# Kernel tuning notes

Hardware: AMD Instinct MI355X
Metric: run time of the kernel (lower is better)

## Reference

```python
import jax, jax.numpy as jnp
import numpy as np

B, T, S = 64, 256, 512          # batch, decode steps, source length
IN, H, P, C = 512, 512, 256, 512  # in_size, rnn hidden, ctx_proj_size, ctx_size


def setup_inputs() -> dict:
    key = jax.random.key(0)
    ks = jax.random.split(key, 10)
    def n(k, sh, s=0.05):
        return jax.random.normal(k, sh, dtype=jnp.float32) * s
    return {
        "dec_input": n(ks[0], (B, T, IN), 1.0),
        "ctx": n(ks[1], (B, S, C), 1.0),
        "ctx_mask": jnp.ones((B, S), jnp.float32),
        # LSTMCell layer 0: input = in_size + ctx_proj_size (input feeding)
        "Wih0": n(ks[2], (4 * H, IN + P)),
        "Whh0": n(ks[3], (4 * H, H)),
        "bih0": jnp.zeros((4 * H,), jnp.float32),
        "bhh0": jnp.zeros((4 * H,), jnp.float32),
        # LSTMCell layer 1
        "Wih1": n(ks[4], (4 * H, H)),
        "Whh1": n(ks[5], (4 * H, H)),
        "bih1": jnp.zeros((4 * H,), jnp.float32),
        "bhh1": jnp.zeros((4 * H,), jnp.float32),
        # bilinear (Luong general) attention weight
        "Watt": n(ks[6], (H, C)),
        # ctx projection: Linear(rnn_size + att.out_features -> ctx_proj_size)
        "Wproj": n(ks[7], (P, H + C)),
        "bproj": jnp.zeros((P,), jnp.float32),
    }


def _lstm_cell(x, h, c, Wih, Whh, bih, bhh):
    # PyTorch LSTMCell gate order: i, f, g, o
    g = x @ Wih.T + bih + h @ Whh.T + bhh
    i, f, gg, o = jnp.split(g, 4, axis=-1)
    c_new = jax.nn.sigmoid(f) * c + jax.nn.sigmoid(i) * jnp.tanh(gg)
    h_new = jax.nn.sigmoid(o) * jnp.tanh(c_new)
    return h_new, c_new


def reference(dec_input, ctx, ctx_mask, Wih0, Whh0, bih0, bhh0,
              Wih1, Whh1, bih1, bhh1, Watt, Wproj, bproj):
    Bn = dec_input.shape[0]
    neg = (ctx_mask - 1.0) * 1e9  # additive mask: 0 where valid, -1e9 where pad

    def step(carry, x_t):
        h0, c0, h1, c1, feed = carry
        # input feeding at layer 0
        x = jnp.concatenate([x_t, feed], axis=1)
        h0, c0 = _lstm_cell(x, h0, c0, Wih0, Whh0, bih0, bhh0)
        h1, c1 = _lstm_cell(h0, h1, c1, Wih1, Whh1, bih1, bhh1)
        # attention on last layer (att_nth_layer == -1)
        q = h1 @ Watt                                   # [B, C]
        score = jnp.einsum('bc,bsc->bs', q, ctx) + neg  # [B, S]
        alpha = jax.nn.softmax(score, axis=-1)
        ectx = jnp.einsum('bs,bsc->bc', alpha, ctx)     # expected context [B, C]
        # ctx projection with tanh (scale_src = scale_tgt = 1.0)
        res = jnp.tanh(jnp.concatenate([h1, ectx], axis=1) @ Wproj.T + bproj)
        return (h0, c0, h1, c1, res), (res, alpha)

    z = lambda d: jnp.zeros((Bn, d), jnp.float32)
    init = (z(H), z(H), z(H), z(H), z(P))
    _, (dec_out, att_w) = jax.lax.scan(step, init, jnp.swapaxes(dec_input, 0, 1))
    # dec_output [B, T, P], attention weights [B, T, S]
    return jnp.swapaxes(dec_out, 0, 1), jnp.swapaxes(att_w, 0, 1)
```

## Files before the change

kernel.cpp:

```cpp
#include <hip/hip_runtime.h>
#include <math.h>

#define B  64
#define T  256
#define S  512
#define IN 512
#define H  512
#define P  256
#define C  512

typedef _Float16 f16x8 __attribute__((ext_vector_type(8)));
typedef float    f32x4 __attribute__((ext_vector_type(4)));
typedef unsigned short u16x8 __attribute__((ext_vector_type(8)));

#define MFMA16(a, b, c) __builtin_amdgcn_mfma_f32_16x16x32_f16(a, b, c, 0, 0, 0)

#define O_C0      0
#define O_C1      131072
#define O_H0F0    262144
#define O_H1F0    524288
#define O_FEEDF   786432
#define O_H1F32   851968
#define O_XF0     983040
#define O_Q       1245184
#define O_PS      1376256
#define O_PSP     1378304
#define O_PEA     1509376
#define O_BCAT0   2557952
#define O_BCAT1   2566144
#define O_WPROJT  2574336
#define O_W0F     3622912
#define O_W1F     14108672
#define O_WATTF   22497280
#define O_CTXH    23545856
#define O_CNTA    57100288
#define O_CNT3    57104384
#define O_H0F1N   57169920
#define O_H1F1N   57300992
#define O_XF1N    57432064

__device__ __forceinline__ float sigm(float x) { return 1.f / (1.f + __expf(-x)); }

__device__ __forceinline__ void split2(float v, unsigned short& hi, unsigned short& lo)
{
    _Float16 h = (_Float16)v;
    float r = (v - (float)h) * 4096.f;
    _Float16 l2 = (_Float16)r;
    union { _Float16 f; unsigned short u; } a, b2;
    a.f = h; b2.f = l2;
    hi = a.u; lo = b2.u;
}

__device__ __forceinline__ unsigned short f2h(float v)
{
    union { _Float16 f; unsigned short u; } x;
    x.f = (_Float16)v;
    return x.u;
}

__device__ __forceinline__ float h2f(unsigned short u)
{
    union { unsigned short u; _Float16 f; } x;
    x.u = u;
    return (float)x.f;
}

__device__ __forceinline__ int frag_us(int r, int k)
{
    return ((((k >> 5) * 4 + (r >> 4)) * 64 + ((k >> 3) & 3) * 16 + (r & 15)) * 16) + (k & 7);
}

__device__ __forceinline__ void gemm_core(
    const unsigned short* A0, int n0, const unsigned short* A1, int n1,
    const unsigned short* A2, const unsigned short* Wf, int nks, int ct,
    float* red, int tid)
{
    const int l = tid & 63, kh = tid >> 6;
    f32x4 acch[4] = {};
    f32x4 accl[4] = {};
    const int KQ = nks >> 3;
#pragma unroll 2
    for (int i = 0; i < KQ; ++i) {
        const int ks = kh * KQ + i;
        const unsigned short* ap; int ksl;
        if (ks < n0)           { ap = A0; ksl = ks; }
        else if (ks < n0 + n1) { ap = A1; ksl = ks - n0; }
        else                   { ap = A2; ksl = ks - n0 - n1; }
        const f16x8* bp = (const f16x8*)(Wf + ((long)(ct * nks + ks) * 64 + l) * 16);
        const f16x8 bh = bp[0];
        const f16x8 bl = bp[1];
#pragma unroll
        for (int mt = 0; mt < 4; ++mt) {
            const f16x8* app = (const f16x8*)(ap + (((ksl * 4 + mt) * 64 + l) * 16));
            const f16x8 ah = app[0];
            const f16x8 al = app[1];
            acch[mt] = MFMA16(ah, bh, acch[mt]);
            accl[mt] = MFMA16(ah, bl, accl[mt]);
            accl[mt] = MFMA16(al, bh, accl[mt]);
        }
    }
#pragma unroll
    for (int mt = 0; mt < 4; ++mt) {
        f32x4 v = acch[mt] + accl[mt] * (1.f / 4096.f);
        *(f32x4*)&red[(kh * 64 + l) * 20 + mt * 4] = v;
    }
}

__device__ __forceinline__ void lstm_epiA(const float* red, unsigned short* stg,
                                          const float* bias, float* cbuf,
                                          float* hf32_atomic, int ct, int tid)
{
    const int b = tid & 63, hl = tid >> 6;
    float g4[4];
#pragma unroll
    for (int g = 0; g < 4; ++g) {
        const int col = hl * 4 + g;
        const int li  = ((b & 15) >> 2) * 16 + col;
        const int ri  = (b >> 4) * 4 + (b & 3);
        float v = bias[ct * 16 + col];
#pragma unroll
        for (int k2 = 0; k2 < 8; ++k2) v += red[(k2 * 64 + li) * 20 + ri];
        g4[g] = v;
    }
    const int hg = ct * 4 + hl;
    const float cold = cbuf[b * H + hg];
    const float cn = sigm(g4[1]) * cold + sigm(g4[0]) * tanhf(g4[2]);
    cbuf[b * H + hg] = cn;
    const float hn = sigm(g4[3]) * tanhf(cn);
    unsigned short hi, lo; split2(hn, hi, lo);
    stg[hl * 64 + b]       = hi;
    stg[256 + hl * 64 + b] = lo;
    if (hf32_atomic) atomicExch(&hf32_atomic[b * H + hg], hn);
}

__device__ __forceinline__ void quad_store(unsigned short* hfrag, int ct,
                                           const unsigned short* stg, int b)
{
    unsigned long long hq = (unsigned long long)stg[b]
        | ((unsigned long long)stg[64 + b]  << 16)
        | ((unsigned long long)stg[128 + b] << 32)
        | ((unsigned long long)stg[192 + b] << 48);
    unsigned long long lq = (unsigned long long)stg[256 + b]
        | ((unsigned long long)stg[320 + b] << 16)
        | ((unsigned long long)stg[384 + b] << 32)
        | ((unsigned long long)stg[448 + b] << 48);
    const int fu0 = frag_us(b, ct * 4);
    atomicExch((unsigned long long*)(hfrag + fu0), hq);
    atomicExch((unsigned long long*)(hfrag + fu0 + 8), lq);
}

__global__ __launch_bounds__(512, 4)
void step_kernel(char* __restrict__ wsb, const float* __restrict__ dec_input,
                 const float* __restrict__ mask, const float* __restrict__ bproj,
                 float* __restrict__ out, int t)
{
    __shared__ char smem[41984];
    const int bid = blockIdx.x, tid = threadIdx.x;
    const int cur = t & 1, nxt = cur ^ 1;

    unsigned short* h0f[2] = {(unsigned short*)(wsb + O_H0F0), (unsigned short*)(wsb + O_H0F1N)};
    unsigned short* h1f[2] = {(unsigned short*)(wsb + O_H1F0), (unsigned short*)(wsb + O_H1F1N)};
    unsigned short* xf[2]  = {(unsigned short*)(wsb + O_XF0),  (unsigned short*)(wsb + O_XF1N)};
    unsigned short* feedf  = (unsigned short*)(wsb + O_FEEDF);
    float* qbuf  = (float*)(wsb + O_Q);
    float* pS    = (float*)(wsb + O_PSP);
    float* Ps    = (float*)(wsb + O_PS);
    float* Pea   = (float*)(wsb + O_PEA);
    float* h1f32 = (float*)(wsb + O_H1F32);
    float* c0    = (float*)(wsb + O_C0);
    float* c1    = (float*)(wsb + O_C1);
    const float* bcat0 = (const float*)(wsb + O_BCAT0);
    const float* bcat1 = (const float*)(wsb + O_BCAT1);
    const float* WprojT = (const float*)(wsb + O_WPROJT);
    const unsigned short* W0f   = (const unsigned short*)(wsb + O_W0F);
    const unsigned short* W1f   = (const unsigned short*)(wsb + O_W1F);
    const unsigned short* Wattf = (const unsigned short*)(wsb + O_WATTF);
    const unsigned short* ctxh  = (const unsigned short*)(wsb + O_CTXH);

    unsigned* cnt1 = (unsigned*)(wsb + O_CNTA) + t;
    unsigned* cnt2 = (unsigned*)(wsb + O_CNTA + 1024) + t;
    unsigned* cntq = (unsigned*)(wsb + O_CNTA + 2048) + t;
    unsigned* cnt3 = (unsigned*)(wsb + O_CNT3) + t * 64;

    float* dec_out = out;
    float* att_out = out + (long)B * T * P;

    float* red = (float*)smem;
    unsigned short* stg = (unsigned short*)(smem + 40960);

    if (bid < 128) {
        gemm_core(xf[cur], 16, feedf, 8, h0f[cur], W0f, 40, bid, red, tid);
        __syncthreads();
        if (tid < 256) lstm_epiA(red, stg, bcat0, c0, nullptr, bid, tid);
        __syncthreads();
        if (tid < 64) quad_store(h0f[nxt], bid, stg, tid);
        __syncthreads();
        if (tid == 0) {
            atomicAdd(cnt1, 1u);
            while (__hip_atomic_load(cnt1, __ATOMIC_RELAXED, __HIP_MEMORY_SCOPE_AGENT) < 128u)
                __builtin_amdgcn_s_sleep(2);
        }
        __syncthreads();
        gemm_core(h0f[nxt], 16, h1f[cur], 16, nullptr, W1f, 32, bid, red, tid);
        __syncthreads();
        if (tid < 256) lstm_epiA(red, stg, bcat1, c1, h1f32, bid, tid);
        __syncthreads();
        if (tid < 64) quad_store(h1f[nxt], bid, stg, tid);
        __syncthreads();
        if (tid == 0) atomicAdd(cnt2, 1u);
        if (bid < 32) {
            if (tid == 0) {
                while (__hip_atomic_load(cnt2, __ATOMIC_RELAXED, __HIP_MEMORY_SCOPE_AGENT) < 128u)
                    __builtin_amdgcn_s_sleep(2);
            }
            __syncthreads();
            gemm_core(h1f[nxt], 16, nullptr, 0, nullptr, Wattf, 16, bid, red, tid);
            __syncthreads();
            if (tid < 256) {
                const int b = tid & 63, cl = tid >> 6;
                float vv[4];
#pragma unroll
                for (int c2 = 0; c2 < 4; ++c2) {
                    const int col = cl * 4 + c2;
                    const int li  = ((b & 15) >> 2) * 16 + col;
                    const int ri  = (b >> 4) * 4 + (b & 3);
                    float v = 0.f;
#pragma unroll
                    for (int k2 = 0; k2 < 8; ++k2) v += red[(k2 * 64 + li) * 20 + ri];
                    vv[c2] = v;
                }
                float* qp = qbuf + b * C + bid * 16 + cl * 4;
                union { float f[2]; unsigned long long u; } p0, p1;
                p0.f[0] = vv[0]; p0.f[1] = vv[1];
                p1.f[0] = vv[2]; p1.f[1] = vv[3];
                atomicExch((unsigned long long*)qp, p0.u);
                atomicExch(((unsigned long long*)qp) + 1, p1.u);
            }
            __syncthreads();
            if (tid == 0) atomicAdd(cntq, 1u);
        }
    } else if (bid < 192) {
        if (t + 1 < T) {
            const int idx = (bid - 128) * 512 + tid;
            const int bb = idx >> 9, k = idx & 511;
            unsigned short hi, lo;
            split2(dec_input[((long)bb * T + (t + 1)) * IN + k], hi, lo);
            unsigned short* dst = xf[nxt];
            const int fu = frag_us(bb, k);
            dst[fu]     = hi;
            dst[fu + 8] = lo;
        }
    }

    if (tid == 0) {
        while (__hip_atomic_load(cntq, __ATOMIC_RELAXED, __HIP_MEMORY_SCOPE_AGENT) < 32u)
            __builtin_amdgcn_s_sleep(8);
    }
    __syncthreads();

    const int ab = bid >> 3, ei = bid & 7;
    {
        float* qs = (float*)smem;
        unsigned short* tile = (unsigned short*)(smem + 2048);
        float* scl = (float*)(smem + 35328);

        if (tid < 128) ((float4*)qs)[tid] = ((const float4*)(qbuf + (long)ab * C))[tid];
        __syncthreads();

        const int row = tid >> 4;
        const int ch  = tid & 15;
        float qv[32];
#pragma unroll
        for (int j = 0; j < 32; ++j) qv[j] = qs[ch * 32 + j];

        const unsigned short* cb16 = ctxh + ((long)ab * S + ei * 64) * C;
        u16x8 creg[4];
#pragma unroll
        for (int it = 0; it < 4; ++it)
            creg[it] = *(const u16x8*)(cb16 + (long)(it * 512 + tid) * 8);

        float eacc = 0.f;
#pragma unroll
        for (int tt = 0; tt < 2; ++tt) {
#pragma unroll
            for (int it = 0; it < 4; ++it) {
                const int i = it * 512 + tid;
                const int r = (i >> 6) & 31, c8 = i & 63;
                *(u16x8*)&tile[r * 520 + c8 * 8] = creg[it];
            }
            __syncthreads();
            if (tt == 0) {
#pragma unroll
                for (int it = 0; it < 4; ++it)
                    creg[it] = *(const u16x8*)(cb16 + 32 * 512 + (long)(it * 512 + tid) * 8);
            }
            float part = 0.f;
#pragma unroll
            for (int j4 = 0; j4 < 4; ++j4) {
                const u16x8 cv = *(const u16x8*)&tile[row * 520 + ch * 32 + j4 * 8];
#pragma unroll
                for (int m = 0; m < 8; ++m)
                    part = fmaf(h2f(cv[m]), qv[j4 * 8 + m], part);
            }
            part += __shfl_xor(part, 1);
            part += __shfl_xor(part, 2);
            part += __shfl_xor(part, 4);
            part += __shfl_xor(part, 8);
            if (ch == 0) {
                const int srow = ei * 64 + tt * 32 + row;
                const float sc = part + (mask[(long)ab * S + srow] - 1.f) * 1e9f;
                const float p  = __expf(sc - 20.f);
                scl[tt * 32 + row] = p;
                atomicExch(&pS[(long)ab * S + srow], p);
            }
            __syncthreads();
#pragma unroll 8
            for (int s = 0; s < 32; ++s)
                eacc = fmaf(scl[tt * 32 + s], h2f(tile[s * 520 + tid]), eacc);
            __syncthreads();
        }

        atomicExch(&Pea[(long)bid * 512 + tid], eacc);
        if (tid < 64) {
            float v = scl[tid];
#pragma unroll
            for (int off = 32; off; off >>= 1) v += __shfl_xor(v, off);
            if (tid == 0) atomicExch(&Ps[bid], v);
        }
    }
    __syncthreads();

    unsigned* shf = (unsigned*)(smem + 35584);
    if (tid == 0) {
        unsigned r = atomicAdd(&cnt3[ab], 1u);
        shf[0] = (r == 7u) ? 1u : 0u;
    }
    __syncthreads();
    if (shf[0]) {
        float* ectx = (float*)smem;
        float* h1l  = (float*)(smem + 2048);
        float* rd3  = (float*)(smem + 4096);

        float gs = 0.f;
#pragma unroll
        for (int j = 0; j < 8; ++j) gs += Ps[ab * 8 + j];
        const float inv = 1.f / gs;

        float v = 0.f;
#pragma unroll
        for (int j = 0; j < 8; ++j) v += Pea[(long)(ab * 8 + j) * 512 + tid];
        ectx[tid] = v * inv;
        h1l[tid]  = h1f32[(long)ab * H + tid];
        att_out[((long)ab * T + t) * S + tid] = pS[(long)ab * S + tid] * inv;
        __syncthreads();

        const int p = tid & 255, half = tid >> 8;
        const float* al = half ? ectx : h1l;
        const float* Wp = WprojT + (long)(half * 512) * P + p;
        float acc = 0.f;
#pragma unroll 8
        for (int kk = 0; kk < 512; ++kk)
            acc = fmaf(al[kk], Wp[(long)kk * P], acc);
        rd3[tid] = acc;
        __syncthreads();

        if (tid < 256) {
            float vv = rd3[tid] + rd3[tid + 256] + bproj[tid];
            vv = tanhf(vv);
            dec_out[((long)ab * T + t) * P + tid] = vv;
            unsigned short hi, lo; split2(vv, hi, lo);
            const int fu = frag_us(ab, tid);
            feedf[fu]     = hi;
            feedf[fu + 8] = lo;
        }
    }
}

__global__ __launch_bounds__(256)
void prep_all(const float* __restrict__ dec_input,
              const float* __restrict__ Wih0, const float* __restrict__ Whh0,
              const float* __restrict__ bih0, const float* __restrict__ bhh0,
              const float* __restrict__ Wih1, const float* __restrict__ Whh1,
              const float* __restrict__ bih1, const float* __restrict__ bhh1,
              const float* __restrict__ Watt, const float* __restrict__ Wproj,
              const float* __restrict__ ctx,
              char* __restrict__ wsb)
{
    const int bid = blockIdx.x, tid = threadIdx.x;
    if (bid < 240) {
        float4 z = {0.f, 0.f, 0.f, 0.f};
        ((float4*)wsb)[bid * 256 + tid] = z;
    } else if (bid < 368) {
        const int idx = (bid - 240) * 256 + tid;
        const int bb = idx >> 9, k = idx & 511;
        unsigned short hi, lo;
        split2(dec_input[((long)bb * T) * IN + k], hi, lo);
        unsigned short* xf0 = (unsigned short*)(wsb + O_XF0);
        const int fu = frag_us(bb, k);
        xf0[fu] = hi; xf0[fu + 8] = lo;
    } else if (bid < 384) {
        const int idx = (bid - 368) * 256 + tid;
        if (idx < 2048) {
            const int p = idx, h = p >> 2, g = p & 3, orig = g * H + h;
            ((float*)(wsb + O_BCAT0))[p] = bih0[orig] + bhh0[orig];
        } else {
            const int p = idx - 2048, h = p >> 2, g = p & 3, orig = g * H + h;
            ((float*)(wsb + O_BCAT1))[p] = bih1[orig] + bhh1[orig];
        }
    } else if (bid < 512) {
        const int idx = (bid - 384) * 256 + tid;
        const int n = idx >> 6, k = (idx & 63) * 8;
        u16x8 hv, lv;
#pragma unroll
        for (int j = 0; j < 8; ++j) {
            unsigned short hi, lo; split2(Watt[(long)(k + j) * C + n], hi, lo);
            hv[j] = hi; lv[j] = lo;
        }
        unsigned short* Wf = (unsigned short*)(wsb + O_WATTF);
        const long base = ((long)((n >> 4) * 16 + (k >> 5)) * 64 + ((k >> 3) & 3) * 16 + (n & 15)) * 16;
        *(u16x8*)(Wf + base)     = hv;
        *(u16x8*)(Wf + base + 8) = lv;
    } else if (bid < 1536) {
        const int idx = (bid - 512) * 256 + tid;
        const int k = idx >> 8, p = idx & 255;
        ((float*)(wsb + O_WPROJT))[k * P + p] = Wproj[(long)p * (H + C) + k];
    } else if (bid < 2816) {
        const int idx = (bid - 1536) * 256 + tid;
        const int n = idx / 160, k8 = idx - n * 160;
        const int k = k8 * 8;
        const int h = n >> 2, g = n & 3, orig = g * H + h;
        const float* src = (k < IN + P) ? (Wih0 + (long)orig * (IN + P) + k)
                                        : (Whh0 + (long)orig * H + (k - (IN + P)));
        u16x8 hv, lv;
#pragma unroll
        for (int j = 0; j < 8; ++j) {
            unsigned short hi, lo; split2(src[j], hi, lo);
            hv[j] = hi; lv[j] = lo;
        }
        unsigned short* Wf = (unsigned short*)(wsb + O_W0F);
        const long base = ((long)((n >> 4) * 40 + (k >> 5)) * 64 + ((k >> 3) & 3) * 16 + (n & 15)) * 16;
        *(u16x8*)(Wf + base)     = hv;
        *(u16x8*)(Wf + base + 8) = lv;
    } else if (bid < 3840) {
        const int idx = (bid - 2816) * 256 + tid;
        const int n = idx >> 7, k = (idx & 127) * 8;
        const int h = n >> 2, g = n & 3, orig = g * H + h;
        const float* src = (k < H) ? (Wih1 + (long)orig * H + k)
                                   : (Whh1 + (long)orig * H + (k - H));
        u16x8 hv, lv;
#pragma unroll
        for (int j = 0; j < 8; ++j) {
            unsigned short hi, lo; split2(src[j], hi, lo);
            hv[j] = hi; lv[j] = lo;
        }
        unsigned short* Wf = (unsigned short*)(wsb + O_W1F);
        const long base = ((long)((n >> 4) * 32 + (k >> 5)) * 64 + ((k >> 3) & 3) * 16 + (n & 15)) * 16;
        *(u16x8*)(Wf + base)     = hv;
        *(u16x8*)(Wf + base + 8) = lv;
    } else if (bid < 7936) {
        const long idx = (long)(bid - 3840) * 256 + tid;
        const float* src = ctx + idx * 16;
        unsigned short* dst = (unsigned short*)(wsb + O_CTXH) + idx * 16;
        u16x8 o0, o1;
#pragma unroll
        for (int j = 0; j < 8; ++j) {
            o0[j] = f2h(src[j]);
            o1[j] = f2h(src[j + 8]);
        }
        *(u16x8*)dst       = o0;
        *(u16x8*)(dst + 8) = o1;
    } else {
        float4 z = {0.f, 0.f, 0.f, 0.f};
        ((float4*)(wsb + O_CNTA))[(bid - 7936) * 256 + tid] = z;
    }
}

extern "C" void kernel_launch(void* const* d_in, const int* in_sizes, int n_in,
                              void* d_out, int out_size, void* d_ws, size_t ws_size,
                              hipStream_t stream)
{
    (void)in_sizes; (void)n_in; (void)out_size; (void)ws_size;
    const float* dec_input = (const float*)d_in[0];
    const float* ctx       = (const float*)d_in[1];
    const float* mask      = (const float*)d_in[2];
    const float* Wih0      = (const float*)d_in[3];
    const float* Whh0      = (const float*)d_in[4];
    const float* bih0      = (const float*)d_in[5];
    const float* bhh0      = (const float*)d_in[6];
    const float* Wih1      = (const float*)d_in[7];
    const float* Whh1      = (const float*)d_in[8];
    const float* bih1      = (const float*)d_in[9];
    const float* bhh1      = (const float*)d_in[10];
    const float* Watt      = (const float*)d_in[11];
    const float* Wproj     = (const float*)d_in[12];
    const float* bproj     = (const float*)d_in[13];
    float* out = (float*)d_out;
    char*  wsb = (char*)d_ws;

    prep_all<<<7953, 256, 0, stream>>>(dec_input, Wih0, Whh0, bih0, bhh0,
                                       Wih1, Whh1, bih1, bhh1, Watt, Wproj,
                                       ctx, wsb);

    for (int t = 0; t < T; ++t)
        step_kernel<<<512, 512, 0, stream>>>(wsb, dec_input, mask, bproj, out, t);
}
```

Measured before the change: 15.05 ms.

## Split attention across 384 blocks and prefetch ctx before waiting on query

The LSTM blocks now also handle the dec_input conversion, and attention work moves to blocks 128+, each handling about 85 source rows (6 blocks per batch row instead of 8). Each block loads its ctx slice into registers and shared memory before spin-waiting on the query counter, so the global load overlaps the recurrent GEMM phase. Shared memory grows to about 69KB, which may lower occupancy and change the grid/launch assumptions. The final reducer now sums 6 partials and reads Ps with atomic loads.

```diff
diff --git a/kernel.cpp b/kernel.cpp
--- a/kernel.cpp
+++ b/kernel.cpp
@@ -154,7 +154,7 @@
                  const float* __restrict__ mask, const float* __restrict__ bproj,
                  float* __restrict__ out, int t)
 {
-    __shared__ char smem[41984];
+    __shared__ char smem[68992];
     const int bid = blockIdx.x, tid = threadIdx.x;
     const int cur = t & 1, nxt = cur ^ 1;
 
@@ -185,10 +185,9 @@
     float* dec_out = out;
     float* att_out = out + (long)B * T * P;
 
-    float* red = (float*)smem;
-    unsigned short* stg = (unsigned short*)(smem + 40960);
-
     if (bid < 128) {
+        float* red = (float*)smem;
+        unsigned short* stg = (unsigned short*)(smem + 40960);
         gemm_core(xf[cur], 16, feedf, 8, h0f[cur], W0f, 40, bid, red, tid);
         __syncthreads();
         if (tid < 256) lstm_epiA(red, stg, bcat0, c0, nullptr, bid, tid);
@@ -238,102 +237,136 @@
             }
             __syncthreads();
             if (tid == 0) atomicAdd(cntq, 1u);
-        }
-    } else if (bid < 192) {
-        if (t + 1 < T) {
-            const int idx = (bid - 128) * 512 + tid;
-            const int bb = idx >> 9, k = idx & 511;
-            unsigned short hi, lo;
-            split2(dec_input[((long)bb * T + (t + 1)) * IN + k], hi, lo);
-            unsigned short* dst = xf[nxt];
-            const int fu = frag_us(bb, k);
-            dst[fu]     = hi;
-            dst[fu + 8] = lo;
-        }
+        } else if (bid < 96) {
+            if (t + 1 < T) {
+                const int idx = (bid - 32) * 512 + tid;
+                const int bb = idx >> 9, k = idx & 511;
+                unsigned short hi, lo;
+                split2(dec_input[((long)bb * T + (t + 1)) * IN + k], hi, lo);
+                unsigned short* dst = xf[nxt];
+                const int fu = frag_us(bb, k);
+                dst[fu]     = hi;
+                dst[fu + 8] = lo;
+            }
+        }
+        return;
+    }
+
+    const int aidx = bid - 128;
+    const int ab = aidx / 6, ei = aidx - ab * 6;
+    const int nr  = (ei < 2) ? 86 : 85;
+    const int sb  = 85 * ei + (ei < 2 ? ei : 2);
+    const int nr1 = nr - 64;
+    const int nel1 = nr1 * 64;
+
+    float* qs = (float*)smem;
+    unsigned short* tile = (unsigned short*)(smem + 2048);
+    float* scl = (float*)(smem + 68608);
+    unsigned* shf = (unsigned*)(smem + 68976);
+
+    const unsigned short* cb16 = ctxh + ((long)ab * S + sb) * C;
+
+    u16x8 c0reg[8];
+#pragma unroll
+    for (int it = 0; it < 8; ++it)
+        c0reg[it] = *(const u16x8*)(cb16 + (long)(it * 512 + tid) * 8);
+    u16x8 c1reg[3];
+#pragma unroll
+    for (int it = 0; it < 3; ++it) {
+        const int i = it * 512 + tid;
+        if (i < nel1) c1reg[it] = *(const u16x8*)(cb16 + 32768 + (long)i * 8);
+    }
+#pragma unroll
+    for (int it = 0; it < 8; ++it) {
+        const int i = it * 512 + tid;
+        *(u16x8*)&tile[(i >> 6) * 520 + (i & 63) * 8] = c0reg[it];
     }
 
     if (tid == 0) {
         while (__hip_atomic_load(cntq, __ATOMIC_RELAXED, __HIP_MEMORY_SCOPE_AGENT) < 32u)
-            __builtin_amdgcn_s_sleep(8);
-    }
-    __syncthreads();
-
-    const int ab = bid >> 3, ei = bid & 7;
-    {
-        float* qs = (float*)smem;
-        unsigned short* tile = (unsigned short*)(smem + 2048);
-        float* scl = (float*)(smem + 35328);
-
-        if (tid < 128) ((float4*)qs)[tid] = ((const float4*)(qbuf + (long)ab * C))[tid];
-        __syncthreads();
-
-        const int row = tid >> 4;
-        const int ch  = tid & 15;
-        float qv[32];
-#pragma unroll
-        for (int j = 0; j < 32; ++j) qv[j] = qs[ch * 32 + j];
-
-        const unsigned short* cb16 = ctxh + ((long)ab * S + ei * 64) * C;
-        u16x8 creg[4];
-#pragma unroll
-        for (int it = 0; it < 4; ++it)
-            creg[it] = *(const u16x8*)(cb16 + (long)(it * 512 + tid) * 8);
-
-        float eacc = 0.f;
-#pragma unroll
-        for (int tt = 0; tt < 2; ++tt) {
-#pragma unroll
-            for (int it = 0; it < 4; ++it) {
-                const int i = it * 512 + tid;
-                const int r = (i >> 6) & 31, c8 = i & 63;
-                *(u16x8*)&tile[r * 520 + c8 * 8] = creg[it];
-            }
-            __syncthreads();
-            if (tt == 0) {
-#pragma unroll
-                for (int it = 0; it < 4; ++it)
-                    creg[it] = *(const u16x8*)(cb16 + 32 * 512 + (long)(it * 512 + tid) * 8);
-            }
-            float part = 0.f;
-#pragma unroll
-            for (int j4 = 0; j4 < 4; ++j4) {
-                const u16x8 cv = *(const u16x8*)&tile[row * 520 + ch * 32 + j4 * 8];
-#pragma unroll
-                for (int m = 0; m < 8; ++m)
-                    part = fmaf(h2f(cv[m]), qv[j4 * 8 + m], part);
-            }
-            part += __shfl_xor(part, 1);
-            part += __shfl_xor(part, 2);
-            part += __shfl_xor(part, 4);
-            part += __shfl_xor(part, 8);
-            if (ch == 0) {
-                const int srow = ei * 64 + tt * 32 + row;
-                const float sc = part + (mask[(long)ab * S + srow] - 1.f) * 1e9f;
-                const float p  = __expf(sc - 20.f);
-                scl[tt * 32 + row] = p;
-                atomicExch(&pS[(long)ab * S + srow], p);
-            }
-            __syncthreads();
+            __builtin_amdgcn_s_sleep(4);
+    }
+    __syncthreads();
+    if (tid < 128) ((float4*)qs)[tid] = ((const float4*)(qbuf + (long)ab * C))[tid];
+    __syncthreads();
+
+    const int row16 = tid >> 4, ch = tid & 15;
+    float qv[32];
+#pragma unroll
+    for (int j = 0; j < 32; ++j) qv[j] = qs[ch * 32 + j];
+
+    float eacc = 0.f;
+#pragma unroll
+    for (int tt = 0; tt < 2; ++tt) {
+        const int r = tt * 32 + row16;
+        float part = 0.f;
+#pragma unroll
+        for (int j4 = 0; j4 < 4; ++j4) {
+            const u16x8 cv = *(const u16x8*)&tile[r * 520 + ch * 32 + j4 * 8];
+#pragma unroll
+            for (int m = 0; m < 8; ++m)
+                part = fmaf(h2f(cv[m]), qv[j4 * 8 + m], part);
+        }
+        part += __shfl_xor(part, 1);
+        part += __shfl_xor(part, 2);
+        part += __shfl_xor(part, 4);
+        part += __shfl_xor(part, 8);
+        if (ch == 0) {
+            const int srow = sb + r;
+            const float sc = part + (mask[(long)ab * S + srow] - 1.f) * 1e9f;
+            const float p  = __expf(sc - 20.f);
+            scl[r] = p;
+            atomicExch(&pS[(long)ab * S + srow], p);
+        }
+    }
+    __syncthreads();
 #pragma unroll 8
-            for (int s = 0; s < 32; ++s)
-                eacc = fmaf(scl[tt * 32 + s], h2f(tile[s * 520 + tid]), eacc);
-            __syncthreads();
-        }
-
-        atomicExch(&Pea[(long)bid * 512 + tid], eacc);
-        if (tid < 64) {
-            float v = scl[tid];
-#pragma unroll
-            for (int off = 32; off; off >>= 1) v += __shfl_xor(v, off);
-            if (tid == 0) atomicExch(&Ps[bid], v);
-        }
-    }
-    __syncthreads();
-
-    unsigned* shf = (unsigned*)(smem + 35584);
+    for (int s = 0; s < 64; ++s)
+        eacc = fmaf(scl[s], h2f(tile[s * 520 + tid]), eacc);
+    __syncthreads();
+#pragma unroll
+    for (int it = 0; it < 3; ++it) {
+        const int i = it * 512 + tid;
+        if (i < nel1) *(u16x8*)&tile[(i >> 6) * 520 + (i & 63) * 8] = c1reg[it];
+    }
+    __syncthreads();
+    if (row16 < nr1) {
+        float part = 0.f;
+#pragma unroll
+        for (int j4 = 0; j4 < 4; ++j4) {
+            const u16x8 cv = *(const u16x8*)&tile[row16 * 520 + ch * 32 + j4 * 8];
+#pragma unroll
+            for (int m = 0; m < 8; ++m)
+                part = fmaf(h2f(cv[m]), qv[j4 * 8 + m], part);
+        }
+        part += __shfl_xor(part, 1);
+        part += __shfl_xor(part, 2);
+        part += __shfl_xor(part, 4);
+        part += __shfl_xor(part, 8);
+        if (ch == 0) {
+            const int srow = sb + 64 + row16;
+            const float sc = part + (mask[(long)ab * S + srow] - 1.f) * 1e9f;
+            const float p  = __expf(sc - 20.f);
+            scl[64 + row16] = p;
+            atomicExch(&pS[(long)ab * S + srow], p);
+        }
+    }
+    __syncthreads();
+    for (int s = 0; s < nr1; ++s)
+        eacc = fmaf(scl[64 + s], h2f(tile[s * 520 + tid]), eacc);
+
+    atomicExch(&Pea[(long)aidx * 512 + tid], eacc);
+    if (tid < 64) {
+        float v = scl[tid] + (tid < nr1 ? scl[64 + tid] : 0.f);
+#pragma unroll
+        for (int off = 32; off; off >>= 1) v += __shfl_xor(v, off);
+        if (tid == 0) atomicExch(&Ps[aidx], v);
+    }
+    __syncthreads();
+
     if (tid == 0) {
         unsigned r = atomicAdd(&cnt3[ab], 1u);
-        shf[0] = (r == 7u) ? 1u : 0u;
+        shf[0] = (r == 5u) ? 1u : 0u;
     }
     __syncthreads();
     if (shf[0]) {
@@ -343,12 +376,13 @@
 
         float gs = 0.f;
 #pragma unroll
-        for (int j = 0; j < 8; ++j) gs += Ps[ab * 8 + j];
+        for (int j = 0; j < 6; ++j)
+            gs += __hip_atomic_load(&Ps[ab * 6 + j], __ATOMIC_RELAXED, __HIP_MEMORY_SCOPE_AGENT);
         const float inv = 1.f / gs;
 
         float v = 0.f;
 #pragma unroll
-        for (int j = 0; j < 8; ++j) v += Pea[(long)(ab * 8 + j) * 512 + tid];
+        for (int j = 0; j < 6; ++j) v += Pea[(long)(ab * 6 + j) * 512 + tid];
         ectx[tid] = v * inv;
         h1l[tid]  = h1f32[(long)ab * H + tid];
         att_out[((long)ab * T + t) * S + tid] = pS[(long)ab * S + tid] * inv;
```

Result: slower. 15.48 ms (+2.9%).

## Give each batch row one attention block with triple-buffered context tiles

Applied to the files above, without the earlier changes.

Attention work moves from 8 blocks per batch row, which merged partial sums through global memory with a counter, to one block per batch row that processes all 512 source positions. It streams context through a three-slot shared-memory ring with register prefetch, and preloads the first tiles before waiting on the query counter. This removes the global partial-sum buffers, the last-block election and the extra atomics. Input conversion moves into the otherwise idle GEMM blocks, and the grid shrinks from 512 to 192 blocks. The trade-off is a much larger shared-memory footprint, lower occupancy, and less parallelism per attention row, since each block now reads its full 512 KB context slice.

```diff
diff --git a/kernel.cpp b/kernel.cpp
--- a/kernel.cpp
+++ b/kernel.cpp
@@ -23,9 +23,6 @@
 #define O_H1F32   851968
 #define O_XF0     983040
 #define O_Q       1245184
-#define O_PS      1376256
-#define O_PSP     1378304
-#define O_PEA     1509376
 #define O_BCAT0   2557952
 #define O_BCAT1   2566144
 #define O_WPROJT  2574336
@@ -34,7 +31,6 @@
 #define O_WATTF   22497280
 #define O_CTXH    23545856
 #define O_CNTA    57100288
-#define O_CNT3    57104384
 #define O_H0F1N   57169920
 #define O_H1F1N   57300992
 #define O_XF1N    57432064
@@ -149,12 +145,12 @@
     atomicExch((unsigned long long*)(hfrag + fu0 + 8), lq);
 }
 
-__global__ __launch_bounds__(512, 4)
+__global__ __launch_bounds__(512, 2)
 void step_kernel(char* __restrict__ wsb, const float* __restrict__ dec_input,
                  const float* __restrict__ mask, const float* __restrict__ bproj,
                  float* __restrict__ out, int t)
 {
-    __shared__ char smem[41984];
+    __shared__ char smem[104192];
     const int bid = blockIdx.x, tid = threadIdx.x;
     const int cur = t & 1, nxt = cur ^ 1;
 
@@ -163,9 +159,6 @@
     unsigned short* xf[2]  = {(unsigned short*)(wsb + O_XF0),  (unsigned short*)(wsb + O_XF1N)};
     unsigned short* feedf  = (unsigned short*)(wsb + O_FEEDF);
     float* qbuf  = (float*)(wsb + O_Q);
-    float* pS    = (float*)(wsb + O_PSP);
-    float* Ps    = (float*)(wsb + O_PS);
-    float* Pea   = (float*)(wsb + O_PEA);
     float* h1f32 = (float*)(wsb + O_H1F32);
     float* c0    = (float*)(wsb + O_C0);
     float* c1    = (float*)(wsb + O_C1);
@@ -180,15 +173,13 @@
     unsigned* cnt1 = (unsigned*)(wsb + O_CNTA) + t;
     unsigned* cnt2 = (unsigned*)(wsb + O_CNTA + 1024) + t;
     unsigned* cntq = (unsigned*)(wsb + O_CNTA + 2048) + t;
-    unsigned* cnt3 = (unsigned*)(wsb + O_CNT3) + t * 64;
 
     float* dec_out = out;
     float* att_out = out + (long)B * T * P;
 
-    float* red = (float*)smem;
-    unsigned short* stg = (unsigned short*)(smem + 40960);
-
     if (bid < 128) {
+        float* red = (float*)smem;
+        unsigned short* stg = (unsigned short*)(smem + 40960);
         gemm_core(xf[cur], 16, feedf, 8, h0f[cur], W0f, 40, bid, red, tid);
         __syncthreads();
         if (tid < 256) lstm_epiA(red, stg, bcat0, c0, nullptr, bid, tid);
@@ -238,141 +229,149 @@
             }
             __syncthreads();
             if (tid == 0) atomicAdd(cntq, 1u);
-        }
-    } else if (bid < 192) {
-        if (t + 1 < T) {
-            const int idx = (bid - 128) * 512 + tid;
-            const int bb = idx >> 9, k = idx & 511;
-            unsigned short hi, lo;
-            split2(dec_input[((long)bb * T + (t + 1)) * IN + k], hi, lo);
-            unsigned short* dst = xf[nxt];
-            const int fu = frag_us(bb, k);
-            dst[fu]     = hi;
-            dst[fu + 8] = lo;
-        }
+        } else if (bid < 96) {
+            if (t + 1 < T) {
+                const int idx = (bid - 32) * 512 + tid;
+                const int bb = idx >> 9, k = idx & 511;
+                unsigned short hi, lo;
+                split2(dec_input[((long)bb * T + (t + 1)) * IN + k], hi, lo);
+                unsigned short* dst = xf[nxt];
+                const int fu = frag_us(bb, k);
+                dst[fu]     = hi;
+                dst[fu + 8] = lo;
+            }
+        }
+        return;
+    }
+
+    const int ab = bid - 128;
+    float* qs  = (float*)smem;
+    unsigned short* tile0 = (unsigned short*)(smem + 2048);
+    float* scl = (float*)(smem + 101888);
+    float* sred = (float*)(smem + 103936);
+
+    const unsigned short* cb16 = ctxh + (long)ab * S * C;
+
+    u16x8 r0[4], r1[4], creg[4];
+#pragma unroll
+    for (int it = 0; it < 4; ++it)
+        r0[it] = *(const u16x8*)(cb16 + (long)(it * 512 + tid) * 8);
+#pragma unroll
+    for (int it = 0; it < 4; ++it)
+        r1[it] = *(const u16x8*)(cb16 + 16384 + (long)(it * 512 + tid) * 8);
+#pragma unroll
+    for (int it = 0; it < 4; ++it)
+        creg[it] = *(const u16x8*)(cb16 + 32768 + (long)(it * 512 + tid) * 8);
+#pragma unroll
+    for (int it = 0; it < 4; ++it) {
+        const int i = it * 512 + tid;
+        *(u16x8*)&tile0[(i >> 6) * 520 + (i & 63) * 8] = r0[it];
+    }
+#pragma unroll
+    for (int it = 0; it < 4; ++it) {
+        const int i = it * 512 + tid;
+        *(u16x8*)&tile0[16640 + (i >> 6) * 520 + (i & 63) * 8] = r1[it];
     }
 
     if (tid == 0) {
         while (__hip_atomic_load(cntq, __ATOMIC_RELAXED, __HIP_MEMORY_SCOPE_AGENT) < 32u)
-            __builtin_amdgcn_s_sleep(8);
+            __builtin_amdgcn_s_sleep(4);
     }
     __syncthreads();
-
-    const int ab = bid >> 3, ei = bid & 7;
-    {
-        float* qs = (float*)smem;
-        unsigned short* tile = (unsigned short*)(smem + 2048);
-        float* scl = (float*)(smem + 35328);
-
-        if (tid < 128) ((float4*)qs)[tid] = ((const float4*)(qbuf + (long)ab * C))[tid];
-        __syncthreads();
-
-        const int row = tid >> 4;
-        const int ch  = tid & 15;
-        float qv[32];
-#pragma unroll
-        for (int j = 0; j < 32; ++j) qv[j] = qs[ch * 32 + j];
-
-        const unsigned short* cb16 = ctxh + ((long)ab * S + ei * 64) * C;
-        u16x8 creg[4];
-#pragma unroll
-        for (int it = 0; it < 4; ++it)
-            creg[it] = *(const u16x8*)(cb16 + (long)(it * 512 + tid) * 8);
-
-        float eacc = 0.f;
-#pragma unroll
-        for (int tt = 0; tt < 2; ++tt) {
+    if (tid < 256) {
+        unsigned long long uq = __hip_atomic_load(
+            (unsigned long long*)(qbuf + (long)ab * C) + tid,
+            __ATOMIC_RELAXED, __HIP_MEMORY_SCOPE_AGENT);
+        union { unsigned long long u; float f[2]; } w; w.u = uq;
+        qs[tid * 2]     = w.f[0];
+        qs[tid * 2 + 1] = w.f[1];
+    }
+    __syncthreads();
+
+    const int row16 = tid >> 4, ch16 = tid & 15;
+    float qv[32];
+#pragma unroll
+    for (int j = 0; j < 32; ++j) qv[j] = qs[ch16 * 32 + j];
+
+    float eacc = 0.f;
+    for (int ch = 0; ch < 16; ++ch) {
+        unsigned short* tc = tile0 + (ch % 3) * 16640;
+        __syncthreads();
+        if (ch + 2 < 16) {
+            unsigned short* tn = tile0 + ((ch + 2) % 3) * 16640;
 #pragma unroll
             for (int it = 0; it < 4; ++it) {
                 const int i = it * 512 + tid;
-                const int r = (i >> 6) & 31, c8 = i & 63;
-                *(u16x8*)&tile[r * 520 + c8 * 8] = creg[it];
+                *(u16x8*)&tn[(i >> 6) * 520 + (i & 63) * 8] = creg[it];
             }
-            __syncthreads();
-            if (tt == 0) {
-#pragma unroll
-                for (int it = 0; it < 4; ++it)
-                    creg[it] = *(const u16x8*)(cb16 + 32 * 512 + (long)(it * 512 + tid) * 8);
-            }
-            float part = 0.f;
-#pragma unroll
-            for (int j4 = 0; j4 < 4; ++j4) {
-                const u16x8 cv = *(const u16x8*)&tile[row * 520 + ch * 32 + j4 * 8];
-#pragma unroll
-                for (int m = 0; m < 8; ++m)
-                    part = fmaf(h2f(cv[m]), qv[j4 * 8 + m], part);
-            }
-            part += __shfl_xor(part, 1);
-            part += __shfl_xor(part, 2);
-            part += __shfl_xor(part, 4);
-            part += __shfl_xor(part, 8);
-            if (ch == 0) {
-                const int srow = ei * 64 + tt * 32 + row;
-                const float sc = part + (mask[(long)ab * S + srow] - 1.f) * 1e9f;
-                const float p  = __expf(sc - 20.f);
-                scl[tt * 32 + row] = p;
-                atomicExch(&pS[(long)ab * S + srow], p);
-            }
-            __syncthreads();
+        }
+        if (ch + 3 < 16) {
+#pragma unroll
+            for (int it = 0; it < 4; ++it)
+                creg[it] = *(const u16x8*)(cb16 + (long)(ch + 3) * 16384 + (long)(it * 512 + tid) * 8);
+        }
+        float part = 0.f;
+#pragma unroll
+        for (int j4 = 0; j4 < 4; ++j4) {
+            const u16x8 cv = *(const u16x8*)&tc[row16 * 520 + ch16 * 32 + j4 * 8];
+#pragma unroll
+            for (int m = 0; m < 8; ++m)
+                part = fmaf(h2f(cv[m]), qv[j4 * 8 + m], part);
+        }
+        part += __shfl_xor(part, 1);
+        part += __shfl_xor(part, 2);
+        part += __shfl_xor(part, 4);
+        part += __shfl_xor(part, 8);
+        if (ch16 == 0) {
+            const int srow = ch * 32 + row16;
+            const float sc = part + (mask[(long)ab * S + srow] - 1.f) * 1e9f;
+            scl[srow] = __expf(sc - 20.f);
+        }
+        __syncthreads();
 #pragma unroll 8
-            for (int s = 0; s < 32; ++s)
-                eacc = fmaf(scl[tt * 32 + s], h2f(tile[s * 520 + tid]), eacc);
-            __syncthreads();
-        }
-
-        atomicExch(&Pea[(long)bid * 512 + tid], eacc);
-        if (tid < 64) {
-            float v = scl[tid];
-#pragma unroll
-            for (int off = 32; off; off >>= 1) v += __shfl_xor(v, off);
-            if (tid == 0) atomicExch(&Ps[bid], v);
-        }
+        for (int s = 0; s < 32; ++s)
+            eacc = fmaf(scl[ch * 32 + s], h2f(tc[s * 520 + tid]), eacc);
     }
     __syncthreads();
 
-    unsigned* shf = (unsigned*)(smem + 35584);
-    if (tid == 0) {
-        unsigned r = atomicAdd(&cnt3[ab], 1u);
-        shf[0] = (r == 7u) ? 1u : 0u;
+    if (tid < 64) {
+        float v = 0.f;
+#pragma unroll
+        for (int k = 0; k < 8; ++k) v += scl[tid + 64 * k];
+#pragma unroll
+        for (int off = 32; off; off >>= 1) v += __shfl_xor(v, off);
+        if (tid == 0) sred[0] = v;
     }
     __syncthreads();
-    if (shf[0]) {
-        float* ectx = (float*)smem;
-        float* h1l  = (float*)(smem + 2048);
-        float* rd3  = (float*)(smem + 4096);
-
-        float gs = 0.f;
-#pragma unroll
-        for (int j = 0; j < 8; ++j) gs += Ps[ab * 8 + j];
-        const float inv = 1.f / gs;
-
-        float v = 0.f;
-#pragma unroll
-        for (int j = 0; j < 8; ++j) v += Pea[(long)(ab * 8 + j) * 512 + tid];
-        ectx[tid] = v * inv;
-        h1l[tid]  = h1f32[(long)ab * H + tid];
-        att_out[((long)ab * T + t) * S + tid] = pS[(long)ab * S + tid] * inv;
-        __syncthreads();
-
-        const int p = tid & 255, half = tid >> 8;
-        const float* al = half ? ectx : h1l;
-        const float* Wp = WprojT + (long)(half * 512) * P + p;
-        float acc = 0.f;
+    const float inv = 1.f / sred[0];
+    att_out[((long)ab * T + t) * S + tid] = scl[tid] * inv;
+
+    float* el  = (float*)(smem + 2048);
+    float* h1l = (float*)(smem + 4096);
+    float* rd3 = (float*)(smem + 6144);
+    el[tid] = eacc * inv;
+    h1l[tid] = __hip_atomic_load(&h1f32[(long)ab * H + tid],
+                                 __ATOMIC_RELAXED, __HIP_MEMORY_SCOPE_AGENT);
+    __syncthreads();
+
+    const int p = tid & 255, half = tid >> 8;
+    const float* al = half ? el : h1l;
+    const float* Wp = WprojT + (long)(half * 512) * P + p;
+    float acc = 0.f;
 #pragma unroll 8
-        for (int kk = 0; kk < 512; ++kk)
-            acc = fmaf(al[kk], Wp[(long)kk * P], acc);
-        rd3[tid] = acc;
-        __syncthreads();
-
-        if (tid < 256) {
-            float vv = rd3[tid] + rd3[tid + 256] + bproj[tid];
-            vv = tanhf(vv);
-            dec_out[((long)ab * T + t) * P + tid] = vv;
-            unsigned short hi, lo; split2(vv, hi, lo);
-            const int fu = frag_us(ab, tid);
-            feedf[fu]     = hi;
-            feedf[fu + 8] = lo;
-        }
+    for (int kk = 0; kk < 512; ++kk)
+        acc = fmaf(al[kk], Wp[(long)kk * P], acc);
+    rd3[tid] = acc;
+    __syncthreads();
+
+    if (tid < 256) {
+        float vv = rd3[tid] + rd3[tid + 256] + bproj[tid];
+        vv = tanhf(vv);
+        dec_out[((long)ab * T + t) * P + tid] = vv;
+        unsigned short hi, lo; split2(vv, hi, lo);
+        const int fu = frag_us(ab, tid);
+        feedf[fu]     = hi;
+        feedf[fu + 8] = lo;
     }
 }
 
@@ -502,5 +501,5 @@
                                        ctx, wsb);
 
     for (int t = 0; t < T; ++t)
-        step_kernel<<<512, 512, 0, stream>>>(wsb, dec_input, mask, bproj, out, t);
-}
+        step_kernel<<<192, 512, 0, stream>>>(wsb, dec_input, mask, bproj, out, t);
+}
```

Result: slower. 18.26 ms (+21.3%).

## Split fused step kernel into three launches replacing spin barriers

Applied to the files above, without the earlier changes.

The single per-step kernel, which used global atomic counters and spin-waits to order the layer-0 LSTM, layer-1 LSTM, query projection and attention phases, is split into three kernels launched back-to-back per timestep. Stream ordering now replaces the cnt1 and cntq spin barriers. The attention kernel issues its ctx prefetch before reading q, and the layer-0 epilogue writes h fragments directly instead of staging them. This removes spin-wait overhead and the tail effects of the 512-block grid all polling, but it triples kernel launch count (768 launches) and adds launch gaps between dependent phases.

```diff
diff --git a/kernel.cpp b/kernel.cpp
--- a/kernel.cpp
+++ b/kernel.cpp
@@ -106,6 +106,33 @@
     }
 }
 
+__device__ __forceinline__ void lstm_epi(const float* red, const float* bias,
+                                         float* cbuf, unsigned short* hfrag,
+                                         int ct, int tid)
+{
+    const int b = tid & 63, hl = tid >> 6;
+    float g4[4];
+#pragma unroll
+    for (int g = 0; g < 4; ++g) {
+        const int col = hl * 4 + g;
+        const int li  = ((b & 15) >> 2) * 16 + col;
+        const int ri  = (b >> 4) * 4 + (b & 3);
+        float v = bias[ct * 16 + col];
+#pragma unroll
+        for (int k2 = 0; k2 < 8; ++k2) v += red[(k2 * 64 + li) * 20 + ri];
+        g4[g] = v;
+    }
+    const int hg = ct * 4 + hl;
+    const float cold = cbuf[b * H + hg];
+    const float cn = sigm(g4[1]) * cold + sigm(g4[0]) * tanhf(g4[2]);
+    cbuf[b * H + hg] = cn;
+    const float hn = sigm(g4[3]) * tanhf(cn);
+    unsigned short hi, lo; split2(hn, hi, lo);
+    const int fu = frag_us(b, hg);
+    hfrag[fu]     = hi;
+    hfrag[fu + 8] = lo;
+}
+
 __device__ __forceinline__ void lstm_epiA(const float* red, unsigned short* stg,
                                           const float* bias, float* cbuf,
                                           float* hf32_atomic, int ct, int tid)
@@ -149,197 +176,182 @@
     atomicExch((unsigned long long*)(hfrag + fu0 + 8), lq);
 }
 
-__global__ __launch_bounds__(512, 4)
-void step_kernel(char* __restrict__ wsb, const float* __restrict__ dec_input,
-                 const float* __restrict__ mask, const float* __restrict__ bproj,
-                 float* __restrict__ out, int t)
-{
-    __shared__ char smem[41984];
+__global__ __launch_bounds__(512)
+void k1_kernel(char* __restrict__ wsb, const float* __restrict__ dec_input, int t)
+{
+    __shared__ float lds[10240];
     const int bid = blockIdx.x, tid = threadIdx.x;
     const int cur = t & 1, nxt = cur ^ 1;
-
+    unsigned short* h0f[2] = {(unsigned short*)(wsb + O_H0F0), (unsigned short*)(wsb + O_H0F1N)};
+    unsigned short* xf[2]  = {(unsigned short*)(wsb + O_XF0),  (unsigned short*)(wsb + O_XF1N)};
+
+    if (bid < 128) {
+        gemm_core(xf[cur], 16, (unsigned short*)(wsb + O_FEEDF), 8, h0f[cur],
+                  (const unsigned short*)(wsb + O_W0F), 40, bid, lds, tid);
+        __syncthreads();
+        if (tid < 256)
+            lstm_epi(lds, (const float*)(wsb + O_BCAT0), (float*)(wsb + O_C0),
+                     h0f[nxt], bid, tid);
+    } else if (t + 1 < T) {
+        const int idx = (bid - 128) * 512 + tid;
+        const int bb = idx >> 9, k = idx & 511;
+        unsigned short hi, lo;
+        split2(dec_input[((long)bb * T + (t + 1)) * IN + k], hi, lo);
+        unsigned short* dst = xf[nxt];
+        const int fu = frag_us(bb, k);
+        dst[fu]     = hi;
+        dst[fu + 8] = lo;
+    }
+}
+
+__global__ __launch_bounds__(512, 2)
+void k2q_kernel(char* __restrict__ wsb, int t)
+{
+    __shared__ float lds[10240];
+    __shared__ unsigned short stg[512];
+    const int bid = blockIdx.x, tid = threadIdx.x;
+    const int cur = t & 1, nxt = cur ^ 1;
     unsigned short* h0f[2] = {(unsigned short*)(wsb + O_H0F0), (unsigned short*)(wsb + O_H0F1N)};
     unsigned short* h1f[2] = {(unsigned short*)(wsb + O_H1F0), (unsigned short*)(wsb + O_H1F1N)};
-    unsigned short* xf[2]  = {(unsigned short*)(wsb + O_XF0),  (unsigned short*)(wsb + O_XF1N)};
-    unsigned short* feedf  = (unsigned short*)(wsb + O_FEEDF);
     float* qbuf  = (float*)(wsb + O_Q);
-    float* pS    = (float*)(wsb + O_PSP);
-    float* Ps    = (float*)(wsb + O_PS);
-    float* Pea   = (float*)(wsb + O_PEA);
-    float* h1f32 = (float*)(wsb + O_H1F32);
-    float* c0    = (float*)(wsb + O_C0);
-    float* c1    = (float*)(wsb + O_C1);
-    const float* bcat0 = (const float*)(wsb + O_BCAT0);
-    const float* bcat1 = (const float*)(wsb + O_BCAT1);
-    const float* WprojT = (const float*)(wsb + O_WPROJT);
-    const unsigned short* W0f   = (const unsigned short*)(wsb + O_W0F);
-    const unsigned short* W1f   = (const unsigned short*)(wsb + O_W1F);
-    const unsigned short* Wattf = (const unsigned short*)(wsb + O_WATTF);
-    const unsigned short* ctxh  = (const unsigned short*)(wsb + O_CTXH);
-
-    unsigned* cnt1 = (unsigned*)(wsb + O_CNTA) + t;
     unsigned* cnt2 = (unsigned*)(wsb + O_CNTA + 1024) + t;
-    unsigned* cntq = (unsigned*)(wsb + O_CNTA + 2048) + t;
+
+    gemm_core(h0f[nxt], 16, h1f[cur], 16, nullptr,
+              (const unsigned short*)(wsb + O_W1F), 32, bid, lds, tid);
+    __syncthreads();
+    if (tid < 256)
+        lstm_epiA(lds, stg, (const float*)(wsb + O_BCAT1), (float*)(wsb + O_C1),
+                  (float*)(wsb + O_H1F32), bid, tid);
+    __syncthreads();
+    if (tid < 64) quad_store(h1f[nxt], bid, stg, tid);
+    __syncthreads();
+    if (tid == 0) atomicAdd(cnt2, 1u);
+
+    if (bid < 32) {
+        if (tid == 0) {
+            while (__hip_atomic_load(cnt2, __ATOMIC_RELAXED, __HIP_MEMORY_SCOPE_AGENT) < 128u)
+                __builtin_amdgcn_s_sleep(2);
+        }
+        __syncthreads();
+        gemm_core(h1f[nxt], 16, nullptr, 0, nullptr,
+                  (const unsigned short*)(wsb + O_WATTF), 16, bid, lds, tid);
+        __syncthreads();
+        if (tid < 256) {
+            const int b = tid & 63, cl = tid >> 6;
+            float4 vv;
+#pragma unroll
+            for (int c2 = 0; c2 < 4; ++c2) {
+                const int col = cl * 4 + c2;
+                const int li  = ((b & 15) >> 2) * 16 + col;
+                const int ri  = (b >> 4) * 4 + (b & 3);
+                float v = 0.f;
+#pragma unroll
+                for (int k2 = 0; k2 < 8; ++k2) v += lds[(k2 * 64 + li) * 20 + ri];
+                ((float*)&vv)[c2] = v;
+            }
+            *(float4*)(qbuf + b * C + bid * 16 + cl * 4) = vv;
+        }
+    }
+}
+
+__global__ __launch_bounds__(512)
+void qattn_mp_kernel(char* __restrict__ wsb, const float* __restrict__ mask,
+                     const float* __restrict__ bproj, float* __restrict__ out, int t)
+{
+    __shared__ float qs[512];
+    __shared__ unsigned short tile[32 * 520];
+    __shared__ float scl[64];
+    __shared__ unsigned shf[1];
+    __shared__ float mrg[1536];
+
+    const int bid = blockIdx.x, tid = threadIdx.x;
+    const int ab = bid >> 3, ei = bid & 7;
+    const float* qbuf = (const float*)(wsb + O_Q);
+    const unsigned short* ctxh = (const unsigned short*)(wsb + O_CTXH);
+    float* pS  = (float*)(wsb + O_PSP);
+    float* Ps  = (float*)(wsb + O_PS);
+    float* Pea = (float*)(wsb + O_PEA);
     unsigned* cnt3 = (unsigned*)(wsb + O_CNT3) + t * 64;
-
     float* dec_out = out;
     float* att_out = out + (long)B * T * P;
 
-    float* red = (float*)smem;
-    unsigned short* stg = (unsigned short*)(smem + 40960);
-
-    if (bid < 128) {
-        gemm_core(xf[cur], 16, feedf, 8, h0f[cur], W0f, 40, bid, red, tid);
-        __syncthreads();
-        if (tid < 256) lstm_epiA(red, stg, bcat0, c0, nullptr, bid, tid);
-        __syncthreads();
-        if (tid < 64) quad_store(h0f[nxt], bid, stg, tid);
-        __syncthreads();
-        if (tid == 0) {
-            atomicAdd(cnt1, 1u);
-            while (__hip_atomic_load(cnt1, __ATOMIC_RELAXED, __HIP_MEMORY_SCOPE_AGENT) < 128u)
-                __builtin_amdgcn_s_sleep(2);
-        }
-        __syncthreads();
-        gemm_core(h0f[nxt], 16, h1f[cur], 16, nullptr, W1f, 32, bid, red, tid);
-        __syncthreads();
-        if (tid < 256) lstm_epiA(red, stg, bcat1, c1, h1f32, bid, tid);
-        __syncthreads();
-        if (tid < 64) quad_store(h1f[nxt], bid, stg, tid);
-        __syncthreads();
-        if (tid == 0) atomicAdd(cnt2, 1u);
-        if (bid < 32) {
-            if (tid == 0) {
-                while (__hip_atomic_load(cnt2, __ATOMIC_RELAXED, __HIP_MEMORY_SCOPE_AGENT) < 128u)
-                    __builtin_amdgcn_s_sleep(2);
-            }
-            __syncthreads();
-            gemm_core(h1f[nxt], 16, nullptr, 0, nullptr, Wattf, 16, bid, red, tid);
-            __syncthreads();
-            if (tid < 256) {
-                const int b = tid & 63, cl = tid >> 6;
-                float vv[4];
-#pragma unroll
-                for (int c2 = 0; c2 < 4; ++c2) {
-                    const int col = cl * 4 + c2;
-                    const int li  = ((b & 15) >> 2) * 16 + col;
-                    const int ri  = (b >> 4) * 4 + (b & 3);
-                    float v = 0.f;
-#pragma unroll
-                    for (int k2 = 0; k2 < 8; ++k2) v += red[(k2 * 64 + li) * 20 + ri];
-                    vv[c2] = v;
-                }
-                float* qp = qbuf + b * C + bid * 16 + cl * 4;
-                union { float f[2]; unsigned long long u; } p0, p1;
-                p0.f[0] = vv[0]; p0.f[1] = vv[1];
-                p1.f[0] = vv[2]; p1.f[1] = vv[3];
-                atomicExch((unsigned long long*)qp, p0.u);
-                atomicExch(((unsigned long long*)qp) + 1, p1.u);
-            }
-            __syncthreads();
-            if (tid == 0) atomicAdd(cntq, 1u);
-        }
-    } else if (bid < 192) {
-        if (t + 1 < T) {
-            const int idx = (bid - 128) * 512 + tid;
-            const int bb = idx >> 9, k = idx & 511;
-            unsigned short hi, lo;
-            split2(dec_input[((long)bb * T + (t + 1)) * IN + k], hi, lo);
-            unsigned short* dst = xf[nxt];
-            const int fu = frag_us(bb, k);
-            dst[fu]     = hi;
-            dst[fu + 8] = lo;
-        }
-    }
-
-    if (tid == 0) {
-        while (__hip_atomic_load(cntq, __ATOMIC_RELAXED, __HIP_MEMORY_SCOPE_AGENT) < 32u)
-            __builtin_amdgcn_s_sleep(8);
-    }
+    const unsigned short* cb16 = ctxh + ((long)ab * S + ei * 64) * C;
+    u16x8 creg[4];
+#pragma unroll
+    for (int it = 0; it < 4; ++it)
+        creg[it] = *(const u16x8*)(cb16 + (long)(it * 512 + tid) * 8);
+
+    if (tid < 128) ((float4*)qs)[tid] = ((const float4*)(qbuf + (long)ab * C))[tid];
     __syncthreads();
 
-    const int ab = bid >> 3, ei = bid & 7;
-    {
-        float* qs = (float*)smem;
-        unsigned short* tile = (unsigned short*)(smem + 2048);
-        float* scl = (float*)(smem + 35328);
-
-        if (tid < 128) ((float4*)qs)[tid] = ((const float4*)(qbuf + (long)ab * C))[tid];
-        __syncthreads();
-
-        const int row = tid >> 4;
-        const int ch  = tid & 15;
-        float qv[32];
-#pragma unroll
-        for (int j = 0; j < 32; ++j) qv[j] = qs[ch * 32 + j];
-
-        const unsigned short* cb16 = ctxh + ((long)ab * S + ei * 64) * C;
-        u16x8 creg[4];
-#pragma unroll
-        for (int it = 0; it < 4; ++it)
-            creg[it] = *(const u16x8*)(cb16 + (long)(it * 512 + tid) * 8);
-
-        float eacc = 0.f;
-#pragma unroll
-        for (int tt = 0; tt < 2; ++tt) {
-#pragma unroll
-            for (int it = 0; it < 4; ++it) {
-                const int i = it * 512 + tid;
-                const int r = (i >> 6) & 31, c8 = i & 63;
-                *(u16x8*)&tile[r * 520 + c8 * 8] = creg[it];
-            }
-            __syncthreads();
-            if (tt == 0) {
-#pragma unroll
-                for (int it = 0; it < 4; ++it)
-                    creg[it] = *(const u16x8*)(cb16 + 32 * 512 + (long)(it * 512 + tid) * 8);
-            }
-            float part = 0.f;
-#pragma unroll
-            for (int j4 = 0; j4 < 4; ++j4) {
-                const u16x8 cv = *(const u16x8*)&tile[row * 520 + ch * 32 + j4 * 8];
-#pragma unroll
-                for (int m = 0; m < 8; ++m)
-                    part = fmaf(h2f(cv[m]), qv[j4 * 8 + m], part);
-            }
-            part += __shfl_xor(part, 1);
-            part += __shfl_xor(part, 2);
-            part += __shfl_xor(part, 4);
-            part += __shfl_xor(part, 8);
-            if (ch == 0) {
-                const int srow = ei * 64 + tt * 32 + row;
-                const float sc = part + (mask[(long)ab * S + srow] - 1.f) * 1e9f;
-                const float p  = __expf(sc - 20.f);
-                scl[tt * 32 + row] = p;
-                atomicExch(&pS[(long)ab * S + srow], p);
-            }
-            __syncthreads();
+    const int row = tid >> 4;
+    const int ch  = tid & 15;
+    float qv[32];
+#pragma unroll
+    for (int j = 0; j < 32; ++j) qv[j] = qs[ch * 32 + j];
+
+    float eacc = 0.f;
+#pragma unroll
+    for (int tt = 0; tt < 2; ++tt) {
+#pragma unroll
+        for (int it = 0; it < 4; ++it) {
+            const int i = it * 512 + tid;
+            const int r = (i >> 6) & 31, c8 = i & 63;
+            *(u16x8*)&tile[r * 520 + c8 * 8] = creg[it];
+        }
+        __syncthreads();
+        if (tt == 0) {
+#pragma unroll
+            for (int it = 0; it < 4; ++it)
+                creg[it] = *(const u16x8*)(cb16 + 32 * 512 + (long)(it * 512 + tid) * 8);
+        }
+        float part = 0.f;
+#pragma unroll
+        for (int j4 = 0; j4 < 4; ++j4) {
+            const u16x8 cv = *(const u16x8*)&tile[row * 520 + ch * 32 + j4 * 8];
+#pragma unroll
+            for (int m = 0; m < 8; ++m)
+                part = fmaf(h2f(cv[m]), qv[j4 * 8 + m], part);
+        }
+        part += __shfl_xor(part, 1);
+        part += __shfl_xor(part, 2);
+        part += __shfl_xor(part, 4);
+        part += __shfl_xor(part, 8);
+        if (ch == 0) {
+            const int srow = ei * 64 + tt * 32 + row;
+            const float sc = part + (mask[(long)ab * S + srow] - 1.f) * 1e9f;
+            const float p  = __expf(sc - 20.f);
+            scl[tt * 32 + row] = p;
+            atomicExch(&pS[(long)ab * S + srow], p);
+        }
+        __syncthreads();
 #pragma unroll 8
-            for (int s = 0; s < 32; ++s)
-                eacc = fmaf(scl[tt * 32 + s], h2f(tile[s * 520 + tid]), eacc);
-            __syncthreads();
-        }
-
-        atomicExch(&Pea[(long)bid * 512 + tid], eacc);
-        if (tid < 64) {
-            float v = scl[tid];
-#pragma unroll
-            for (int off = 32; off; off >>= 1) v += __shfl_xor(v, off);
-            if (tid == 0) atomicExch(&Ps[bid], v);
-        }
+        for (int s = 0; s < 32; ++s)
+            eacc = fmaf(scl[tt * 32 + s], h2f(tile[s * 520 + tid]), eacc);
+        __syncthreads();
+    }
+
+    atomicExch(&Pea[(long)bid * 512 + tid], eacc);
+    if (tid < 64) {
+        float v = scl[tid];
+#pragma unroll
+        for (int off = 32; off; off >>= 1) v += __shfl_xor(v, off);
+        if (tid == 0) atomicExch(&Ps[bid], v);
     }
     __syncthreads();
 
-    unsigned* shf = (unsigned*)(smem + 35584);
     if (tid == 0) {
         unsigned r = atomicAdd(&cnt3[ab], 1u);
         shf[0] = (r == 7u) ? 1u : 0u;
     }
     __syncthreads();
     if (shf[0]) {
-        float* ectx = (float*)smem;
-        float* h1l  = (float*)(smem + 2048);
-        float* rd3  = (float*)(smem + 4096);
+        float* ectx = mrg;
+        float* h1l  = mrg + 512;
+        float* rd3  = mrg + 1024;
+        const float* h1f32 = (const float*)(wsb + O_H1F32);
+        const float* WprojT = (const float*)(wsb + O_WPROJT);
+        unsigned short* feedf = (unsigned short*)(wsb + O_FEEDF);
 
         float gs = 0.f;
 #pragma unroll
@@ -501,6 +513,9 @@
                                        Wih1, Whh1, bih1, bhh1, Watt, Wproj,
                                        ctx, wsb);
 
-    for (int t = 0; t < T; ++t)
-        step_kernel<<<512, 512, 0, stream>>>(wsb, dec_input, mask, bproj, out, t);
-}
+    for (int t = 0; t < T; ++t) {
+        k1_kernel<<<192, 512, 0, stream>>>(wsb, dec_input, t);
+        k2q_kernel<<<128, 512, 0, stream>>>(wsb, t);
+        qattn_mp_kernel<<<512, 512, 0, stream>>>(wsb, mask, bproj, out, t);
+    }
+}
```

Result: no change. 15.26 ms (+1.4%).
